# Kernel optimization log

Measured on AMD Instinct MI355X. Metric: run time of the kernel, lower is better.

## Reference

```python
import jax, jax.numpy as jnp
import numpy as np
from jax import lax

GAMMA = 1.0   # soft-min temperature (init kwarg)
BIG = 1e10    # finite stand-in for +inf (safe gradients, exp(-BIG/gamma) == 0 in fp32)


def _pairwise_sqdist(X, Z):
    # X: (N, T, d), Z: (T, d) -> D: (N, T, T) squared Euclidean, without (N,T,T,d) intermediate
    x2 = jnp.sum(X * X, axis=-1)              # (N, T)
    z2 = jnp.sum(Z * Z, axis=-1)              # (T,)
    xz = jnp.einsum('ntd,sd->nts', X, Z)      # (N, T, T)
    return x2[:, :, None] + z2[None, None, :] - 2.0 * xz


def _softdtw_batch(D, gamma):
    # D: (N, T, T) cost matrices. Anti-diagonal wavefront DP:
    #   R[i,j] = D[i,j] + softmin(R[i-1,j], R[i,j-1], R[i-1,j-1]),  R[0,0]=0, borders=BIG
    # Diagonal k = i + j (i,j in 1..T); diagonal arrays indexed by ii = i-1 in [0, T).
    N, T, _ = D.shape
    ii = jnp.arange(T)
    inv_g = 1.0 / gamma

    def softmin(a, b, c):
        s = jnp.stack([a, b, c], axis=0) * (-inv_g)
        return -gamma * jax.scipy.special.logsumexp(s, axis=0)

    def step(carry, k):
        d_prev2, d_prev1 = carry              # diagonals k-2 and k-1, each (N, T)
        jj = k - 2 - ii                        # column index j-1 for row index ii
        valid = (jj >= 0) & (jj < T)
        dvals = jnp.take_along_axis(
            D, jnp.clip(jj, 0, T - 1)[None, :, None], axis=2)[..., 0]  # (N, T)
        r_left = d_prev1                                   # R[i, j-1]
        r_up = jnp.concatenate(
            [jnp.full((N, 1), BIG, D.dtype), d_prev1[:, :-1]], axis=1)  # R[i-1, j]
        corner = jnp.where(k == 2, jnp.asarray(0.0, D.dtype), jnp.asarray(BIG, D.dtype))
        r_diag = jnp.concatenate(
            [jnp.broadcast_to(corner, (N, 1)), d_prev2[:, :-1]], axis=1)  # R[i-1, j-1]
        new_d = jnp.where(valid[None, :], dvals + softmin(r_up, r_left, r_diag),
                          jnp.asarray(BIG, D.dtype))
        return (d_prev1, new_d), None

    d0 = jnp.full((N, T), BIG, D.dtype)
    (_, last), _ = lax.scan(step, (d0, d0), jnp.arange(2, 2 * T + 1))
    return last[:, T - 1]                      # R[T, T] per sample


def setup_inputs() -> dict:
    key = jax.random.key(0)
    k1, k2, k3 = jax.random.split(key, 3)
    N, T, d = 64, 512, 16
    X = jax.random.normal(k1, (N, T, d), dtype=jnp.float32)
    weights = jax.random.uniform(k2, (N,), dtype=jnp.float32)
    Z = jax.random.normal(k3, (T, d), dtype=jnp.float32)
    return {"X": X, "weights": weights, "Z": Z}


def reference(X, weights, Z):
    D = _pairwise_sqdist(X, Z)                 # (N, T, T)
    sdtw = _softdtw_batch(D, GAMMA)            # (N,)
    return jnp.sum(weights * sdtw)             # scalar barycenter loss
```

## Files before the change

### kernel.cpp

```cpp
#include <hip/hip_runtime.h>

#define TT 512
#define BIGS 1.4426950408889634e10f
#define LOG2E 1.4426950408889634f
#define M2L  (-2.0f * 1.4426950408889634f)
#define LN2F 0.69314718055994531f
#define P_SS 16
#define G_LAG 96
#define N_SS 54
#define RSTR 130

typedef _Float16 h2 __attribute__((ext_vector_type(2)));

__device__ __forceinline__ unsigned pk(float a, float b) {
    h2 v; v.x = (_Float16)a; v.y = (_Float16)b;
    return __builtin_bit_cast(unsigned, v);
}

#if __has_builtin(__builtin_amdgcn_fdot2)
#define FDOT2(a, b, c) __builtin_amdgcn_fdot2(__builtin_bit_cast(h2, (a)), \
                                              __builtin_bit_cast(h2, (b)), (c), false)
#else
__device__ __forceinline__ float fdot2_sw(unsigned a, unsigned b, float c) {
    h2 ha = __builtin_bit_cast(h2, a), hb = __builtin_bit_cast(h2, b);
    return c + (float)ha.x * (float)hb.x + (float)ha.y * (float)hb.y;
}
#define FDOT2(a, b, c) fdot2_sw((a), (b), (c))
#endif

#if __has_builtin(__builtin_amdgcn_exp2f)
#define EXP2F(x) __builtin_amdgcn_exp2f(x)
#else
#define EXP2F(x) exp2f(x)
#endif

#define ZROW(jv) (((((jv) & 1)) << 8) | ((((jv) >> 1)) & 255))

__device__ __forceinline__ float dppshr1(float x, float old) {
#if __has_builtin(__builtin_amdgcn_update_dpp)
    return __builtin_bit_cast(float,
        __builtin_amdgcn_update_dpp(__builtin_bit_cast(int, old),
                                    __builtin_bit_cast(int, x),
                                    0x138 , 0xF, 0xF, false));
#else
    const float v = __shfl_up(x, 1);
    return ((threadIdx.x & 63) == 0) ? old : v;
#endif
}

__global__ __launch_bounds__(768, 1) void k_fused(const float* __restrict__ X,
                                                  const float* __restrict__ Z,
                                                  const float* __restrict__ w,
                                                  float* __restrict__ out) {
    const int tt = threadIdx.x;
    const int t  = tt & 63;
    const int wv = tt >> 6;
    const int bd = wv & 3;
    const int hf = (wv >= 8) ? 1 : 0;
    const int n  = blockIdx.x;

    __shared__ uint4    ZA[2][512];
    __shared__ float    Zs2p[512];
    __shared__ float2   seam[4][64];
    __shared__ unsigned ring[4][64][RSTR];

    if (tt < 512) {
        const int r = tt;
        const float4* zp = (const float4*)(Z + (size_t)r * 16);
        const float4 a0 = zp[0], a1 = zp[1], a2 = zp[2], a3 = zp[3];
        float sv = 0.0f;
        sv = fmaf(a0.x, a0.x, sv); sv = fmaf(a0.y, a0.y, sv);
        sv = fmaf(a0.z, a0.z, sv); sv = fmaf(a0.w, a0.w, sv);
        sv = fmaf(a1.x, a1.x, sv); sv = fmaf(a1.y, a1.y, sv);
        sv = fmaf(a1.z, a1.z, sv); sv = fmaf(a1.w, a1.w, sv);
        sv = fmaf(a2.x, a2.x, sv); sv = fmaf(a2.y, a2.y, sv);
        sv = fmaf(a2.z, a2.z, sv); sv = fmaf(a2.w, a2.w, sv);
        sv = fmaf(a3.x, a3.x, sv); sv = fmaf(a3.y, a3.y, sv);
        sv = fmaf(a3.z, a3.z, sv); sv = fmaf(a3.w, a3.w, sv);
        const int idx = ((r & 1) << 8) | (r >> 1);
        ZA[0][idx] = make_uint4(pk(a0.x, a0.y), pk(a0.z, a0.w),
                                pk(a1.x, a1.y), pk(a1.z, a1.w));
        ZA[1][idx] = make_uint4(pk(a2.x, a2.y), pk(a2.z, a2.w),
                                pk(a3.x, a3.y), pk(a3.z, a3.w));
        Zs2p[idx] = LOG2E * sv;
    }
    if (tt < 256) ((float2*)&seam[0][0])[tt] = make_float2(BIGS, 1.0f);

    const int i0 = 128 * bd + 2 * t;
    unsigned Xu[2][8];
    float    xs2[2];
    const float* xp = X + ((size_t)n * TT + i0) * 16;
#pragma unroll
    for (int q = 0; q < 2; ++q) {
        const float4* xr = (const float4*)(xp + q * 16);
        const float4 a0 = xr[0], a1 = xr[1], a2 = xr[2], a3 = xr[3];
        float sv = 0.0f;
        sv = fmaf(a0.x, a0.x, sv); sv = fmaf(a0.y, a0.y, sv);
        sv = fmaf(a0.z, a0.z, sv); sv = fmaf(a0.w, a0.w, sv);
        sv = fmaf(a1.x, a1.x, sv); sv = fmaf(a1.y, a1.y, sv);
        sv = fmaf(a1.z, a1.z, sv); sv = fmaf(a1.w, a1.w, sv);
        sv = fmaf(a2.x, a2.x, sv); sv = fmaf(a2.y, a2.y, sv);
        sv = fmaf(a2.z, a2.z, sv); sv = fmaf(a2.w, a2.w, sv);
        sv = fmaf(a3.x, a3.x, sv); sv = fmaf(a3.y, a3.y, sv);
        sv = fmaf(a3.z, a3.z, sv); sv = fmaf(a3.w, a3.w, sv);
        xs2[q] = LOG2E * sv;
        Xu[q][0] = pk(a0.x, a0.y); Xu[q][1] = pk(a0.z, a0.w);
        Xu[q][2] = pk(a1.x, a1.y); Xu[q][3] = pk(a1.z, a1.w);
        Xu[q][4] = pk(a2.x, a2.y); Xu[q][5] = pk(a2.z, a2.w);
        Xu[q][6] = pk(a3.x, a3.y); Xu[q][7] = pk(a3.z, a3.w);
    }
    const float wgt = w[n];
    const float2* rKS = &seam[bd][0];
    unsigned* const rg = &ring[bd][t][0];
    __syncthreads();

#define PRODUCE(Tv)                                                           \
    {                                                                         \
        const int base_ = ((Tv) << 4) + (hf << 3);                            \
        const int wb_ = base_ & 127;                                          \
        _Pragma("unroll 4")                                                   \
        for (int cc = 0; cc < 8; ++cc) {                                      \
            const int zr = ZROW(base_ + cc);                \
            const uint4 z0 = ZA[0][zr], z1 = ZA[1][zr];                       \
            const float zz = Zs2p[zr];                                        \
            float a0 = 0.0f, b0 = 0.0f, a1 = 0.0f, b1 = 0.0f;                 \
            a0 = FDOT2(z0.x, Xu[0][0], a0); a0 = FDOT2(z0.y, Xu[0][1], a0);   \
            a0 = FDOT2(z0.z, Xu[0][2], a0); a0 = FDOT2(z0.w, Xu[0][3], a0);   \
            b0 = FDOT2(z1.x, Xu[0][4], b0); b0 = FDOT2(z1.y, Xu[0][5], b0);   \
            b0 = FDOT2(z1.z, Xu[0][6], b0); b0 = FDOT2(z1.w, Xu[0][7], b0);   \
            a1 = FDOT2(z0.x, Xu[1][0], a1); a1 = FDOT2(z0.y, Xu[1][1], a1);   \
            a1 = FDOT2(z0.z, Xu[1][2], a1); a1 = FDOT2(z0.w, Xu[1][3], a1);   \
            b1 = FDOT2(z1.x, Xu[1][4], b1); b1 = FDOT2(z1.y, Xu[1][5], b1);   \
            b1 = FDOT2(z1.z, Xu[1][6], b1); b1 = FDOT2(z1.w, Xu[1][7], b1);   \
            const float dd0 = fmaf(M2L, a0 + b0, xs2[0] + zz);                \
            const float dd1 = fmaf(M2L, a1 + b1, xs2[1] + zz);                \
            rg[wb_ + cc] = pk(dd0, dd1);                                      \
        }                                                                     \
    }

    if (wv >= 4 && bd == 0) { PRODUCE(0) PRODUCE(1) }
    __syncthreads();

    float RpK[2], RpS[2], poK, poS_s, bnK, bnS;
    float E[2][6];
    float sprevS_d;
    unsigned rv[2];
    RpK[0] = RpK[1] = BIGS; RpS[0] = RpS[1] = 1.0f;
    poK = BIGS; poS_s = 1.0f; bnK = BIGS; bnS = 1.0f;
    sprevS_d = 1.0f;
    rv[0] = rv[1] = 0u;
#pragma unroll
    for (int e = 0; e < 6; ++e) { E[0][e] = 1.0f; E[1][e] = 1.0f; }

#define LTICK(q, tl, ALLOK)                                                   \
    {                                                                         \
        const float K1_d = RpK[1];            \
        const float2 sprev = rKS[((tl) + 1) & 63];                            \
        const h2 dh = __builtin_bit_cast(h2, rv[q]);                          \
        rv[q] = rg[((unsigned)((tl) + 2 - t)) & 127];      \
        const float dd0 = (float)dh.x, dd1 = (float)dh.y;                     \
                 \
        const float unK = bnK;                                                \
        const float pK  = poK;                                                \
        const float l0K = RpK[0], l1K = RpK[1];                               \
        const float m0 = fminf(fminf(unK, l0K), pK);                          \
        const float K0 = dd0 + m0;                                            \
        const float m1 = fminf(fminf(K0, l1K), l0K);                          \
        const float K1 = dd1 + m1;                                            \
        const bool okK = (ALLOK) ? true                                       \
                       : ((((tl) - t) >= 0) && (((tl) - t) < 512));           \
        RpK[0] = okK ? K0 : RpK[0];                                           \
        RpK[1] = okK ? K1 : RpK[1];                                           \
        poK = unK;                                                            \
                  \
        E[q][0] = EXP2F(m0 - unK);                                            \
        E[q][1] = EXP2F(m0 - l0K);                                            \
        E[q][2] = EXP2F(m0 - pK);                                             \
        E[q][3] = EXP2F(m1 - K0);                                             \
        E[q][4] = EXP2F(m1 - l1K);                                            \
        E[q][5] = EXP2F(m1 - l0K);                                            \
          \
        const bool okS = (ALLOK) ? true                                       \
                       : ((((tl) - 1 - t) >= 0) && (((tl) - 1 - t) < 512));   \
        const float s0 = E[(q) ^ 1][0] * bnS + E[(q) ^ 1][1] * RpS[0]         \
                       + E[(q) ^ 1][2] * poS_s;                               \
        const float s1 = E[(q) ^ 1][3] * s0 + E[(q) ^ 1][4] * RpS[1]          \
                       + E[(q) ^ 1][5] * RpS[0];                              \
        RpS[0] = okS ? s0 : RpS[0];                                           \
        RpS[1] = okS ? s1 : RpS[1];                                           \
        if (okS && bd < 3 && t == 63) {   \
            seam[bd + 1][(tl) & 63] = make_float2(K1_d, RpS[1]);              \
        }                                                                     \
        poS_s = bnS;                                \
                                                 \
        bnK = dppshr1(RpK[1], sprev.x);               \
        bnS = dppshr1(RpS[1], sprevS_d);              \
        sprevS_d = sprev.y;                                                   \
    }

#define RENORM                                                                \
    {                                                                         \
        _Pragma("unroll")                                                     \
        for (int q = 0; q < 2; ++q) {                                         \
            const int e = (int)(__float_as_uint(RpS[q]) >> 23) - 127;         \
            RpS[q] = __uint_as_float(__float_as_uint(RpS[q])                  \
                                     - ((unsigned)e << 23));                  \
            RpK[q] -= (float)e;                                               \
        }                                                                     \
    }

#define SS_BODY(A)                                                            \
    LTICK(0, tb + 0, A)  LTICK(1, tb + 1, A)  LTICK(0, tb + 2, A)             \
    LTICK(1, tb + 3, A)  LTICK(0, tb + 4, A)  LTICK(1, tb + 5, A)             \
    LTICK(0, tb + 6, A)  LTICK(1, tb + 7, A)                                  \
    RENORM                                                                    \
    LTICK(0, tb + 8, A)  LTICK(1, tb + 9, A)  LTICK(0, tb + 10, A)            \
    LTICK(1, tb + 11, A) LTICK(0, tb + 12, A) LTICK(1, tb + 13, A)            \
    LTICK(0, tb + 14, A) LTICK(1, tb + 15, A)                                 \
    RENORM

#pragma unroll 1
    for (int s = 0; s < N_SS; ++s) {
        if (wv >= 4) {
            const int T = s - 6 * bd + 2;
            if (T >= 0 && T <= 31) PRODUCE(T)
        } else {
            const int tb = P_SS * s - G_LAG * bd;
            if (tb >= 64 && tb <= 496) {
                __builtin_amdgcn_s_setprio(1);
                SS_BODY(1)
                __builtin_amdgcn_s_setprio(0);
            } else if (tb >= 0 && tb <= 574) {
                if (tb == 0) {
                    RpK[0] = RpK[1] = BIGS; RpS[0] = RpS[1] = 1.0f;
                    poK = (bd == 0 && t == 0) ? 0.0f : BIGS;
                    poS_s = 1.0f;
                    const float2 r0 = rKS[0];
                    bnK = r0.x;
                    bnS = 1.0f;
                    sprevS_d = r0.y;
                    rv[0] = rg[((unsigned)(0 - t)) & 127];
                    rv[1] = rg[((unsigned)(1 - t)) & 127];
                }
                __builtin_amdgcn_s_setprio(1);
                SS_BODY(0)
                __builtin_amdgcn_s_setprio(0);
            }
        }
        __syncthreads();
    }
#undef LTICK
#undef RENORM
#undef SS_BODY
#undef PRODUCE

    if (wv == 3 && t == 63) {
        atomicAdd(out, wgt * (RpK[1] - log2f(RpS[1])) * LN2F);
    }
}

__global__ void k_zero(float* out) {
    if (threadIdx.x == 0) out[0] = 0.0f;
}

extern "C" void kernel_launch(void* const* d_in, const int* in_sizes, int n_in,
                              void* d_out, int out_size, void* d_ws, size_t ws_size,
                              hipStream_t stream) {
    const float* X = (const float*)d_in[0];
    const float* w = (const float*)d_in[1];
    const float* Z = (const float*)d_in[2];
    float* out = (float*)d_out;

    hipLaunchKernelGGL(k_zero, dim3(1), dim3(64), 0, stream, out);
    hipLaunchKernelGGL(k_fused, dim3(64), dim3(768), 0, stream, X, Z, w, out);
}
```

Baseline: 167.9 us.

## Replace lockstep block barriers with LDS progress-flag point-to-point sync

Replaces the global superstep loop, which ran a __syncthreads after every 16-tick step, with per-wave progress counters in shared memory. Each DP wave spins on its neighbour's and its producers' counters, and producers spin on their consumer DP wave. This removes block-wide barrier stalls and lets waves run ahead by as much as their dependencies allow. The cost is spin-wait polling with s_sleep, and the code relies on volatile LDS ordering being correct.

```diff
diff --git a/kernel.cpp b/kernel.cpp
--- a/kernel.cpp
+++ b/kernel.cpp
@@ -5,9 +5,6 @@
 #define LOG2E 1.4426950408889634f
 #define M2L  (-2.0f * 1.4426950408889634f)
 #define LN2F 0.69314718055994531f
-#define P_SS 16
-#define G_LAG 96
-#define N_SS 54
 #define RSTR 130
 
 typedef _Float16 h2 __attribute__((ext_vector_type(2)));
@@ -48,6 +45,15 @@
 #endif
 }
 
+__device__ __forceinline__ void waitge(const volatile int* p, int v) {
+    while (*p < v) __builtin_amdgcn_s_sleep(2);
+    asm volatile("" ::: "memory");
+}
+__device__ __forceinline__ void waitge2(const volatile int* p, int v) {
+    while (p[0] < v || p[1] < v) __builtin_amdgcn_s_sleep(2);
+    asm volatile("" ::: "memory");
+}
+
 __global__ __launch_bounds__(768, 1) void k_fused(const float* __restrict__ X,
                                                   const float* __restrict__ Z,
                                                   const float* __restrict__ w,
@@ -63,6 +69,8 @@
     __shared__ float    Zs2p[512];
     __shared__ float2   seam[4][64];
     __shared__ unsigned ring[4][64][RSTR];
+    __shared__ int      dpProg[4];
+    __shared__ int      prodProg[4][2];
 
     if (tt < 512) {
         const int r = tt;
@@ -85,6 +93,8 @@
         Zs2p[idx] = LOG2E * sv;
     }
     if (tt < 256) ((float2*)&seam[0][0])[tt] = make_float2(BIGS, 1.0f);
+    if (tt < 4) dpProg[tt] = 0;
+    if (tt < 8) (&prodProg[0][0])[tt] = 0;
 
     const int i0 = 128 * bd + 2 * t;
     unsigned Xu[2][8];
@@ -137,9 +147,6 @@
             rg[wb_ + cc] = pk(dd0, dd1);                                      \
         }                                                                     \
     }
-
-    if (wv >= 4 && bd == 0) { PRODUCE(0) PRODUCE(1) }
-    __syncthreads();
 
     float RpK[2], RpS[2], poK, poS_s, bnK, bnS;
     float E[2][6];
@@ -219,35 +226,50 @@
     LTICK(0, tb + 14, A) LTICK(1, tb + 15, A)                                 \
     RENORM
 
+    if (wv < 4) {
 #pragma unroll 1
-    for (int s = 0; s < N_SS; ++s) {
-        if (wv >= 4) {
-            const int T = s - 6 * bd + 2;
-            if (T >= 0 && T <= 31) PRODUCE(T)
-        } else {
-            const int tb = P_SS * s - G_LAG * bd;
-            if (tb >= 64 && tb <= 496) {
-                __builtin_amdgcn_s_setprio(1);
+        for (int k = 0; k < 36; ++k) {
+            const int tb = k << 4;
+            if (bd > 0) {
+                const int tgt = (tb + 96 < 576) ? tb + 96 : 576;
+                waitge(&dpProg[bd - 1], tgt);
+            }
+            if (bd < 3 && k >= 8) {
+                waitge(&dpProg[bd + 1], tb - 112);
+            }
+            {
+                const int tw = (k + 2 < 32) ? k + 2 : 32;
+                waitge2(&prodProg[bd][0], tw);
+            }
+            __builtin_amdgcn_s_setprio(1);
+            if (k == 0) {
+                RpK[0] = RpK[1] = BIGS; RpS[0] = RpS[1] = 1.0f;
+                poK = (bd == 0 && t == 0) ? 0.0f : BIGS;
+                poS_s = 1.0f;
+                const float2 r0 = rKS[0];
+                bnK = r0.x;
+                bnS = 1.0f;
+                sprevS_d = r0.y;
+                rv[0] = rg[((unsigned)(0 - t)) & 127];
+                rv[1] = rg[((unsigned)(1 - t)) & 127];
+                SS_BODY(0)
+            } else if (k >= 4 && k <= 31) {
                 SS_BODY(1)
-                __builtin_amdgcn_s_setprio(0);
-            } else if (tb >= 0 && tb <= 574) {
-                if (tb == 0) {
-                    RpK[0] = RpK[1] = BIGS; RpS[0] = RpS[1] = 1.0f;
-                    poK = (bd == 0 && t == 0) ? 0.0f : BIGS;
-                    poS_s = 1.0f;
-                    const float2 r0 = rKS[0];
-                    bnK = r0.x;
-                    bnS = 1.0f;
-                    sprevS_d = r0.y;
-                    rv[0] = rg[((unsigned)(0 - t)) & 127];
-                    rv[1] = rg[((unsigned)(1 - t)) & 127];
-                }
-                __builtin_amdgcn_s_setprio(1);
+            } else {
                 SS_BODY(0)
-                __builtin_amdgcn_s_setprio(0);
-            }
+            }
+            __builtin_amdgcn_s_setprio(0);
+            asm volatile("s_waitcnt lgkmcnt(0)" ::: "memory");
+            if (t == 0) *(volatile int*)&dpProg[bd] = tb + 16;
         }
-        __syncthreads();
+    } else {
+#pragma unroll 1
+        for (int T = 0; T < 32; ++T) {
+            if (T >= 4) waitge(&dpProg[bd], (T << 4) - 48);
+            PRODUCE(T)
+            asm volatile("s_waitcnt lgkmcnt(0)" ::: "memory");
+            if (t == 0) *(volatile int*)&prodProg[bd][hf] = T + 1;
+        }
     }
 #undef LTICK
 #undef RENORM
```

Result: no change. 165.1 us (-1.7%).
